# Kernel optimization log

Measured on AMD Instinct MI355X. Metric: run time of the kernel, lower is better.

## Reference

```python
import jax, jax.numpy as jnp
import numpy as np

B, T, U, D = 32, 128, 768, 768


def setup_inputs() -> dict:
    key = jax.random.key(0)
    ks = jax.random.split(key, 8)
    s = 0.02  # init scale for kernels (glorot-ish for 768)
    return {
        "x": jax.random.normal(ks[0], (B, T, D), jnp.float32),
        "h0": jax.random.normal(ks[1], (B, U), jnp.float32) * 0.1,
        "kernel": jax.random.normal(ks[2], (U, D), jnp.float32) * s,
        "recurrent_kernel": jax.random.normal(ks[3], (U, U), jnp.float32) * s,
        "attention_kernel": jax.random.normal(ks[4], (U, D), jnp.float32) * s,
        "recurrent_attention_kernel": jax.random.normal(ks[5], (U, U), jnp.float32) * s,
        "bias": jnp.zeros((U,), jnp.float32),
        "gamma_prime_attention": jnp.float32(-1.0),
        "gamma_prime_recurrent_attention": jnp.float32(-1.0),
    }


def _cell(x_t, h, kernel, rk, ak, rak, bias, ga, gra):
    # x_t: [B,D], h: [B,U]
    # input cross-attention: outer(h, x_t) * ak, exp, row-normalize, gate by kernel
    att = jnp.exp(h[:, :, None] * x_t[:, None, :] * ak)          # [B,U,D]
    att = att / jnp.sum(att, axis=-1, keepdims=True)
    att = att * kernel                                            # [B,U,D]
    hh = x_t @ kernel.T                                           # [B,U]
    hh = hh + ga * jnp.einsum('bud,bd->bu', att, x_t)
    hh = hh + bias
    # recurrent self-attention: outer(h, h) * rak, exp, row-normalize, gate by rk
    ratt = jnp.exp(h[:, :, None] * h[:, None, :] * rak)           # [B,U,U]
    ratt = ratt / jnp.sum(ratt, axis=-1, keepdims=True)
    ratt = ratt * rk
    out = hh + h @ rk.T + gra * jnp.einsum('buv,bv->bu', ratt, h)
    return jnp.tanh(out)


def reference(x, h0, kernel, recurrent_kernel, attention_kernel,
              recurrent_attention_kernel, bias,
              gamma_prime_attention, gamma_prime_recurrent_attention):
    ga = jax.nn.sigmoid(gamma_prime_attention)
    gra = jax.nn.sigmoid(gamma_prime_recurrent_attention)

    def step(h, x_t):
        o = _cell(x_t, h, kernel, recurrent_kernel, attention_kernel,
                  recurrent_attention_kernel, bias, ga, gra)
        return o, o

    _, ys = jax.lax.scan(step, h0, jnp.swapaxes(x, 0, 1))  # ys: [T,B,U]
    return jnp.swapaxes(ys, 0, 1)  # [B,T,U]
```

## Files before the change

### kernel.cpp

```cpp
#include <hip/hip_runtime.h>

#define NB 32
#define NT 128
#define NU 768
#define ND 768
#define UPB 3
#define NBLK (NU / UPB)
#define NTHR (256 * UPB)

#define AGENT __HIP_MEMORY_SCOPE_AGENT

__device__ __forceinline__ float fexp2(float x) { return __builtin_amdgcn_exp2f(x); }
__device__ __forceinline__ float frcp(float x)  { return __builtin_amdgcn_rcpf(x); }

__global__ void transpose_x_kernel(const float* __restrict__ x, float* __restrict__ xT) {
  __shared__ float tile[32][33];
  const int t  = blockIdx.x;
  const int d0 = blockIdx.y * 32;
  const int lo = threadIdx.x & 31;
  const int hi = threadIdx.x >> 5;
#pragma unroll
  for (int bb = hi; bb < 32; bb += 8)
    tile[bb][lo] = x[((size_t)bb * NT + t) * ND + d0 + lo];
  __syncthreads();
#pragma unroll
  for (int dd = hi; dd < 32; dd += 8)
    xT[((size_t)t * ND + d0 + dd) * NB + lo] = tile[lo][dd];
}

__global__ void init_h_kernel(const float* __restrict__ h0, float* __restrict__ hT,
                              unsigned int* __restrict__ flags) {
  int i = blockIdx.x * 256 + threadIdx.x;
  if (i < NU * NB) hT[i] = h0[(i & 31) * NU + (i >> 5)];
  if (i < NBLK) flags[i] = 0u;
}

__global__ void transpose_out_kernel(const float* __restrict__ outT, float* __restrict__ out) {
  __shared__ float tile[32][33];
  const int t  = blockIdx.x;
  const int u0 = blockIdx.y * 32;
  const int lo = threadIdx.x & 31;
  const int hi = threadIdx.x >> 5;
#pragma unroll
  for (int uu = hi; uu < 32; uu += 8)
    tile[uu][lo] = outT[((size_t)t * NU + u0 + uu) * NB + lo];
  __syncthreads();
#pragma unroll
  for (int bb = hi; bb < 32; bb += 8)
    out[((size_t)bb * NT + t) * NU + u0 + lo] = tile[lo][bb];
}

__global__ void __launch_bounds__(NTHR)
rnn_fused_kernel(const float* __restrict__ xT,
                 const float* __restrict__ wk,
                 const float* __restrict__ wrk,
                 const float* __restrict__ wak,
                 const float* __restrict__ wrak,
                 const float* __restrict__ bias,
                 const float* __restrict__ gpa,
                 const float* __restrict__ gpra,
                 float* hA, float* hB,
                 float* __restrict__ outT,
                 unsigned int* flags)
{
  const int tid  = threadIdx.x;
  const int uloc = tid >> 8;
  const int lt   = tid & 255;
  const int b    = lt & 31;
  const int c    = lt >> 5;
  const int d0   = c * 96;
  const int u    = blockIdx.x * UPB + uloc;

  __shared__ float2 s2a[UPB][ND];
  __shared__ float2 s2r[UPB][ND];
  __shared__ float  red[UPB][6][4][32];

#pragma unroll
  for (int j = 0; j < UPB; ++j) {
    const int ug = blockIdx.x * UPB + j;
    s2a[j][tid] = make_float2(wak [(size_t)ug * ND + tid], wk [(size_t)ug * ND + tid]);
    s2r[j][tid] = make_float2(wrak[(size_t)ug * NU + tid], wrk[(size_t)ug * NU + tid]);
  }
  const float bias_u = bias[u];
  const float ga  = 1.0f / (1.0f + __expf(-gpa[0]));
  const float gra = 1.0f / (1.0f + __expf(-gpra[0]));
  __syncthreads();

  float* hcur  = hA;
  float* hnext = hB;
  const float LOG2E = 1.4426950408889634f;

  for (int t = 0; t < NT; ++t) {
    const float hu = __hip_atomic_load(&hcur[u * NB + b], __ATOMIC_RELAXED, AGENT);
    const float hs = hu * LOG2E;

    float s_a = 0.f, n_a = 0.f, l_a = 0.f;
    {
      const float*  xp = xT + ((size_t)t * ND + d0) * NB + b;
      const float2* wa = &s2a[uloc][d0];
#pragma unroll 8
      for (int k = 0; k < 96; ++k) {
        float2 w2 = wa[k];
        float  xv = xp[k * NB];
        float  e  = fexp2(hs * xv * w2.x);
        float  kx = w2.y * xv;
        s_a += e;
        l_a += kx;
        n_a = fmaf(e, kx, n_a);
      }
    }
    float s_r = 0.f, n_r = 0.f, l_r = 0.f;
    {
      float*        hp = hcur + (size_t)d0 * NB + b;
      const float2* wr = &s2r[uloc][d0];
#pragma unroll 8
      for (int k = 0; k < 96; ++k) {
        float2 w2 = wr[k];
        float  hv = __hip_atomic_load(&hp[k * NB], __ATOMIC_RELAXED, AGENT);
        float  e  = fexp2(hs * hv * w2.x);
        float  kh = w2.y * hv;
        s_r += e;
        l_r += kh;
        n_r = fmaf(e, kh, n_r);
      }
    }

    float v0 = s_a + __shfl_xor(s_a, 32);
    float v1 = n_a + __shfl_xor(n_a, 32);
    float v2 = l_a + __shfl_xor(l_a, 32);
    float v3 = s_r + __shfl_xor(s_r, 32);
    float v4 = n_r + __shfl_xor(n_r, 32);
    float v5 = l_r + __shfl_xor(l_r, 32);
    const int w = (tid >> 6) & 3;
    if ((tid & 63) < 32) {
      red[uloc][0][w][b] = v0; red[uloc][1][w][b] = v1; red[uloc][2][w][b] = v2;
      red[uloc][3][w][b] = v3; red[uloc][4][w][b] = v4; red[uloc][5][w][b] = v5;
    }
    __syncthreads();

    if (lt < 32) {
      float r0 = red[uloc][0][0][b] + red[uloc][0][1][b] + red[uloc][0][2][b] + red[uloc][0][3][b];
      float r1 = red[uloc][1][0][b] + red[uloc][1][1][b] + red[uloc][1][2][b] + red[uloc][1][3][b];
      float r2 = red[uloc][2][0][b] + red[uloc][2][1][b] + red[uloc][2][2][b] + red[uloc][2][3][b];
      float r3 = red[uloc][3][0][b] + red[uloc][3][1][b] + red[uloc][3][2][b] + red[uloc][3][3][b];
      float r4 = red[uloc][4][0][b] + red[uloc][4][1][b] + red[uloc][4][2][b] + red[uloc][4][3][b];
      float r5 = red[uloc][5][0][b] + red[uloc][5][1][b] + red[uloc][5][2][b] + red[uloc][5][3][b];
      float hh = r2 + bias_u + ga * (r1 * frcp(r0));
      float z  = hh + r5 + gra * (r4 * frcp(r3));
      float ex = fexp2(z * 2.8853900817779268f);
      float o  = 1.0f - 2.0f * frcp(ex + 1.0f);
      __hip_atomic_store(&hnext[u * NB + b], o, __ATOMIC_RELAXED, AGENT);
      outT[((size_t)t * NU + u) * NB + b] = o;
    }

    if (t != NT - 1) {
      asm volatile("s_waitcnt vmcnt(0)" ::: "memory");
      __syncthreads();
      if (tid == 0)
        __hip_atomic_store(&flags[blockIdx.x], (unsigned)(t + 1), __ATOMIC_RELAXED, AGENT);
      if (tid < NBLK) {
        const unsigned tgt = (unsigned)(t + 1);
        while (__hip_atomic_load(&flags[tid], __ATOMIC_RELAXED, AGENT) < tgt)
          __builtin_amdgcn_s_sleep(2);
      }
      __syncthreads();
    }
    { float* tmp = hcur; hcur = hnext; hnext = tmp; }
  }
}

extern "C" void kernel_launch(void* const* d_in, const int* in_sizes, int n_in,
                              void* d_out, int out_size, void* d_ws, size_t ws_size,
                              hipStream_t stream) {
  const float* x    = (const float*)d_in[0];
  const float* h0   = (const float*)d_in[1];
  const float* wk   = (const float*)d_in[2];
  const float* wrk  = (const float*)d_in[3];
  const float* wak  = (const float*)d_in[4];
  const float* wrak = (const float*)d_in[5];
  const float* bias = (const float*)d_in[6];
  const float* gpa  = (const float*)d_in[7];
  const float* gpra = (const float*)d_in[8];
  float* out = (float*)d_out;

  float* xT   = (float*)d_ws;
  float* outT = xT + (size_t)NT * ND * NB;
  float* hA   = outT + (size_t)NT * NU * NB;
  float* hB   = hA + NU * NB;
  unsigned int* flags = (unsigned int*)(hB + NU * NB);

  transpose_x_kernel<<<dim3(NT, ND / 32), 256, 0, stream>>>(x, xT);
  init_h_kernel<<<(NU * NB + 255) / 256, 256, 0, stream>>>(h0, hA, flags);
  rnn_fused_kernel<<<NBLK, NTHR, 0, stream>>>(xT, wk, wrk, wak, wrak, bias, gpa, gpra,
                                              hA, hB, outT, flags);
  transpose_out_kernel<<<dim3(NT, NU / 32), 256, 0, stream>>>(outT, out);
}
```

Baseline: 1.997 ms.

## Stage hidden state in LDS per step and vectorize the inner loops

Each step, the block now cooperatively loads the whole hidden state (stored batch-major) into padded shared memory with dwordx4 loads that bypass stale cache (sc1). The inner loop then reads h from LDS instead of issuing per-element atomic global loads. x is also relaid out so each thread reads contiguous 96-float chunks, and the weights are split into separate arrays, so the two attention loops fuse into one loop using 128-bit loads. This is meant to cut global-memory latency on the critical serial recurrence, at the cost of about 99KB of extra LDS and a full per-step h broadcast into every block.

```diff
diff --git a/kernel.cpp b/kernel.cpp
--- a/kernel.cpp
+++ b/kernel.cpp
@@ -7,31 +7,28 @@
 #define UPB 3
 #define NBLK (NU / UPB)
 #define NTHR (256 * UPB)
+#define HPAD 772
 
 #define AGENT __HIP_MEMORY_SCOPE_AGENT
+
+typedef float f32x4 __attribute__((ext_vector_type(4)));
 
 __device__ __forceinline__ float fexp2(float x) { return __builtin_amdgcn_exp2f(x); }
 __device__ __forceinline__ float frcp(float x)  { return __builtin_amdgcn_rcpf(x); }
 
-__global__ void transpose_x_kernel(const float* __restrict__ x, float* __restrict__ xT) {
-  __shared__ float tile[32][33];
-  const int t  = blockIdx.x;
-  const int d0 = blockIdx.y * 32;
-  const int lo = threadIdx.x & 31;
-  const int hi = threadIdx.x >> 5;
-#pragma unroll
-  for (int bb = hi; bb < 32; bb += 8)
-    tile[bb][lo] = x[((size_t)bb * NT + t) * ND + d0 + lo];
-  __syncthreads();
-#pragma unroll
-  for (int dd = hi; dd < 32; dd += 8)
-    xT[((size_t)t * ND + d0 + dd) * NB + lo] = tile[lo][dd];
+__global__ void make_xc_kernel(const float* __restrict__ x, float* __restrict__ xc) {
+  const int t = blockIdx.x;
+  const int c = blockIdx.y;
+  for (int e = threadIdx.x; e < 32 * 96; e += 256) {
+    int b = e / 96, k = e - b * 96;
+    xc[(((size_t)t * 8 + c) * 32) * 96 + e] = x[((size_t)b * NT + t) * ND + c * 96 + k];
+  }
 }
 
 __global__ void init_h_kernel(const float* __restrict__ h0, float* __restrict__ hT,
                               unsigned int* __restrict__ flags) {
   int i = blockIdx.x * 256 + threadIdx.x;
-  if (i < NU * NB) hT[i] = h0[(i & 31) * NU + (i >> 5)];
+  if (i < NU * NB) hT[i] = h0[i];
   if (i < NBLK) flags[i] = 0u;
 }
 
@@ -50,8 +47,8 @@
     out[((size_t)bb * NT + t) * NU + u0 + lo] = tile[lo][bb];
 }
 
-__global__ void __launch_bounds__(NTHR)
-rnn_fused_kernel(const float* __restrict__ xT,
+__global__ void __launch_bounds__(NTHR, 3)
+rnn_fused_kernel(const float* __restrict__ xc,
                  const float* __restrict__ wk,
                  const float* __restrict__ wrk,
                  const float* __restrict__ wak,
@@ -59,7 +56,7 @@
                  const float* __restrict__ bias,
                  const float* __restrict__ gpa,
                  const float* __restrict__ gpra,
-                 float* hA, float* hB,
+                 float* hTA, float* hTB,
                  float* __restrict__ outT,
                  unsigned int* flags)
 {
@@ -71,57 +68,72 @@
   const int d0   = c * 96;
   const int u    = blockIdx.x * UPB + uloc;
 
-  __shared__ float2 s2a[UPB][ND];
-  __shared__ float2 s2r[UPB][ND];
-  __shared__ float  red[UPB][6][4][32];
+  __shared__ __align__(16) float s_ak[UPB][ND], s_k[UPB][ND], s_rak[UPB][ND], s_rk[UPB][ND];
+  __shared__ __align__(16) float sh[NB * HPAD];
+  __shared__ float red[UPB][6][4][32];
 
 #pragma unroll
   for (int j = 0; j < UPB; ++j) {
     const int ug = blockIdx.x * UPB + j;
-    s2a[j][tid] = make_float2(wak [(size_t)ug * ND + tid], wk [(size_t)ug * ND + tid]);
-    s2r[j][tid] = make_float2(wrak[(size_t)ug * NU + tid], wrk[(size_t)ug * NU + tid]);
+    s_ak [j][tid] = wak [(size_t)ug * ND + tid];
+    s_k  [j][tid] = wk  [(size_t)ug * ND + tid];
+    s_rak[j][tid] = wrak[(size_t)ug * NU + tid];
+    s_rk [j][tid] = wrk [(size_t)ug * NU + tid];
   }
   const float bias_u = bias[u];
   const float ga  = 1.0f / (1.0f + __expf(-gpa[0]));
   const float gra = 1.0f / (1.0f + __expf(-gpra[0]));
-  __syncthreads();
-
-  float* hcur  = hA;
-  float* hnext = hB;
+
+  const int tq = tid / 192;
+  const int ur = 4 * tid - 768 * tq;
+
+  const float* hcurT = hTA;
+  float* hnextT = hTB;
   const float LOG2E = 1.4426950408889634f;
 
   for (int t = 0; t < NT; ++t) {
-    const float hu = __hip_atomic_load(&hcur[u * NB + b], __ATOMIC_RELAXED, AGENT);
+    f32x4 hr[8];
+#pragma unroll
+    for (int j = 0; j < 8; ++j) {
+      const float* p = hcurT + j * 3072 + 4 * tid;
+      asm volatile("global_load_dwordx4 %0, %1, off sc1"
+                   : "=&v"(hr[j]) : "v"(p) : "memory");
+    }
+    asm volatile("s_waitcnt vmcnt(0)" ::: "memory");
+    __builtin_amdgcn_sched_barrier(0);
+#pragma unroll
+    for (int j = 0; j < 8; ++j)
+      *(f32x4*)&sh[(4 * j + tq) * HPAD + ur] = hr[j];
+    __syncthreads();
+
+    const float hu = sh[b * HPAD + u];
     const float hs = hu * LOG2E;
 
     float s_a = 0.f, n_a = 0.f, l_a = 0.f;
-    {
-      const float*  xp = xT + ((size_t)t * ND + d0) * NB + b;
-      const float2* wa = &s2a[uloc][d0];
-#pragma unroll 8
-      for (int k = 0; k < 96; ++k) {
-        float2 w2 = wa[k];
-        float  xv = xp[k * NB];
-        float  e  = fexp2(hs * xv * w2.x);
-        float  kx = w2.y * xv;
-        s_a += e;
-        l_a += kx;
-        n_a = fmaf(e, kx, n_a);
-      }
-    }
     float s_r = 0.f, n_r = 0.f, l_r = 0.f;
-    {
-      float*        hp = hcur + (size_t)d0 * NB + b;
-      const float2* wr = &s2r[uloc][d0];
-#pragma unroll 8
-      for (int k = 0; k < 96; ++k) {
-        float2 w2 = wr[k];
-        float  hv = __hip_atomic_load(&hp[k * NB], __ATOMIC_RELAXED, AGENT);
-        float  e  = fexp2(hs * hv * w2.x);
-        float  kh = w2.y * hv;
-        s_r += e;
-        l_r += kh;
-        n_r = fmaf(e, kh, n_r);
+    const float* xp  = xc + ((size_t)(t * 8 + c) * 32 + b) * 96;
+    const float* hp  = &sh[b * HPAD + d0];
+    const float* ap  = &s_ak [uloc][d0];
+    const float* kp  = &s_k  [uloc][d0];
+    const float* rap = &s_rak[uloc][d0];
+    const float* rkp = &s_rk [uloc][d0];
+
+#pragma unroll 4
+    for (int k4 = 0; k4 < 24; ++k4) {
+      f32x4 xv  = *(const f32x4*)(xp  + 4 * k4);
+      f32x4 hv  = *(const f32x4*)(hp  + 4 * k4);
+      f32x4 av  = *(const f32x4*)(ap  + 4 * k4);
+      f32x4 kv  = *(const f32x4*)(kp  + 4 * k4);
+      f32x4 rav = *(const f32x4*)(rap + 4 * k4);
+      f32x4 rkv = *(const f32x4*)(rkp + 4 * k4);
+#pragma unroll
+      for (int j = 0; j < 4; ++j) {
+        float e  = fexp2(hs * xv[j] * av[j]);
+        float kx = kv[j] * xv[j];
+        s_a += e; l_a += kx; n_a = fmaf(e, kx, n_a);
+        float er = fexp2(hs * hv[j] * rav[j]);
+        float kh = rkv[j] * hv[j];
+        s_r += er; l_r += kh; n_r = fmaf(er, kh, n_r);
       }
     }
 
@@ -149,7 +161,7 @@
       float z  = hh + r5 + gra * (r4 * frcp(r3));
       float ex = fexp2(z * 2.8853900817779268f);
       float o  = 1.0f - 2.0f * frcp(ex + 1.0f);
-      __hip_atomic_store(&hnext[u * NB + b], o, __ATOMIC_RELAXED, AGENT);
+      __hip_atomic_store(&hnextT[b * NU + u], o, __ATOMIC_RELAXED, AGENT);
       outT[((size_t)t * NU + u) * NB + b] = o;
     }
 
@@ -165,7 +177,7 @@
       }
       __syncthreads();
     }
-    { float* tmp = hcur; hcur = hnext; hnext = tmp; }
+    { const float* tmp = hcurT; hcurT = hnextT; hnextT = (float*)tmp; }
   }
 }
 
@@ -183,15 +195,15 @@
   const float* gpra = (const float*)d_in[8];
   float* out = (float*)d_out;
 
-  float* xT   = (float*)d_ws;
-  float* outT = xT + (size_t)NT * ND * NB;
-  float* hA   = outT + (size_t)NT * NU * NB;
-  float* hB   = hA + NU * NB;
-  unsigned int* flags = (unsigned int*)(hB + NU * NB);
-
-  transpose_x_kernel<<<dim3(NT, ND / 32), 256, 0, stream>>>(x, xT);
-  init_h_kernel<<<(NU * NB + 255) / 256, 256, 0, stream>>>(h0, hA, flags);
-  rnn_fused_kernel<<<NBLK, NTHR, 0, stream>>>(xT, wk, wrk, wak, wrak, bias, gpa, gpra,
-                                              hA, hB, outT, flags);
+  float* xc   = (float*)d_ws;
+  float* outT = xc + (size_t)NT * ND * NB;
+  float* hTA  = outT + (size_t)NT * NU * NB;
+  float* hTB  = hTA + NU * NB;
+  unsigned int* flags = (unsigned int*)(hTB + NU * NB);
+
+  make_xc_kernel<<<dim3(NT, 8), 256, 0, stream>>>(x, xc);
+  init_h_kernel<<<(NU * NB + 255) / 256, 256, 0, stream>>>(h0, hTA, flags);
+  rnn_fused_kernel<<<NBLK, NTHR, 0, stream>>>(xc, wk, wrk, wak, wrak, bias, gpa, gpra,
+                                              hTA, hTB, outT, flags);
   transpose_out_kernel<<<dim3(NT, NU / 32), 256, 0, stream>>>(outT, out);
 }
```

After: 2.202 ms. 10.3% more time.

## Split the batch across two blocks per unit group to double block count

Applied to the files above, without the earlier changes.

Each group of three hidden units is now handled by two blocks, one per half of the batch, giving 512 blocks in total. Each thread reduces over 48 features instead of 96, and an extra shuffle stage folds the sixteen chunks. This halves the serial work per thread at every time step, which is meant to shorten the per-step critical path. In exchange the grid-wide flag barrier now polls 512 flags, each block loads the full weight rows, global loads are only 16 floats wide, and all 512 blocks must be co-resident or the spin barrier deadlocks.

```diff
diff --git a/kernel.cpp b/kernel.cpp
--- a/kernel.cpp
+++ b/kernel.cpp
@@ -5,8 +5,10 @@
 #define NU 768
 #define ND 768
 #define UPB 3
-#define NBLK (NU / UPB)
-#define NTHR (256 * UPB)
+#define NC 16
+#define CL 48
+#define NBLK 512
+#define NTHR 768
 
 #define AGENT __HIP_MEMORY_SCOPE_AGENT
 
@@ -50,7 +52,7 @@
     out[((size_t)bb * NT + t) * NU + u0 + lo] = tile[lo][bb];
 }
 
-__global__ void __launch_bounds__(NTHR)
+__global__ void __launch_bounds__(NTHR, 6)
 rnn_fused_kernel(const float* __restrict__ xT,
                  const float* __restrict__ wk,
                  const float* __restrict__ wrk,
@@ -63,21 +65,24 @@
                  float* __restrict__ outT,
                  unsigned int* flags)
 {
-  const int tid  = threadIdx.x;
-  const int uloc = tid >> 8;
-  const int lt   = tid & 255;
-  const int b    = lt & 31;
-  const int c    = lt >> 5;
-  const int d0   = c * 96;
-  const int u    = blockIdx.x * UPB + uloc;
+  const int tid   = threadIdx.x;
+  const int uloc  = tid >> 8;
+  const int lt    = tid & 255;
+  const int b     = lt & 15;
+  const int c     = lt >> 4;
+  const int d0    = c * CL;
+  const int ugrp  = blockIdx.x >> 1;
+  const int bhalf = blockIdx.x & 1;
+  const int u     = ugrp * UPB + uloc;
+  const int bg    = bhalf * 16 + b;
 
   __shared__ float2 s2a[UPB][ND];
   __shared__ float2 s2r[UPB][ND];
-  __shared__ float  red[UPB][6][4][32];
+  __shared__ float  red[UPB][6][4][16];
 
 #pragma unroll
   for (int j = 0; j < UPB; ++j) {
-    const int ug = blockIdx.x * UPB + j;
+    const int ug = ugrp * UPB + j;
     s2a[j][tid] = make_float2(wak [(size_t)ug * ND + tid], wk [(size_t)ug * ND + tid]);
     s2r[j][tid] = make_float2(wrak[(size_t)ug * NU + tid], wrk[(size_t)ug * NU + tid]);
   }
@@ -91,66 +96,62 @@
   const float LOG2E = 1.4426950408889634f;
 
   for (int t = 0; t < NT; ++t) {
-    const float hu = __hip_atomic_load(&hcur[u * NB + b], __ATOMIC_RELAXED, AGENT);
+    const float hu = __hip_atomic_load(&hcur[u * NB + bg], __ATOMIC_RELAXED, AGENT);
     const float hs = hu * LOG2E;
 
     float s_a = 0.f, n_a = 0.f, l_a = 0.f;
     {
-      const float*  xp = xT + ((size_t)t * ND + d0) * NB + b;
+      const float*  xp = xT + ((size_t)t * ND + d0) * NB + bg;
       const float2* wa = &s2a[uloc][d0];
 #pragma unroll 8
-      for (int k = 0; k < 96; ++k) {
+      for (int k = 0; k < CL; ++k) {
         float2 w2 = wa[k];
         float  xv = xp[k * NB];
         float  e  = fexp2(hs * xv * w2.x);
         float  kx = w2.y * xv;
-        s_a += e;
-        l_a += kx;
-        n_a = fmaf(e, kx, n_a);
+        s_a += e; l_a += kx; n_a = fmaf(e, kx, n_a);
       }
     }
     float s_r = 0.f, n_r = 0.f, l_r = 0.f;
     {
-      float*        hp = hcur + (size_t)d0 * NB + b;
+      float*        hp = hcur + (size_t)d0 * NB + bg;
       const float2* wr = &s2r[uloc][d0];
 #pragma unroll 8
-      for (int k = 0; k < 96; ++k) {
+      for (int k = 0; k < CL; ++k) {
         float2 w2 = wr[k];
         float  hv = __hip_atomic_load(&hp[k * NB], __ATOMIC_RELAXED, AGENT);
         float  e  = fexp2(hs * hv * w2.x);
         float  kh = w2.y * hv;
-        s_r += e;
-        l_r += kh;
-        n_r = fmaf(e, kh, n_r);
+        s_r += e; l_r += kh; n_r = fmaf(e, kh, n_r);
       }
     }
 
-    float v0 = s_a + __shfl_xor(s_a, 32);
-    float v1 = n_a + __shfl_xor(n_a, 32);
-    float v2 = l_a + __shfl_xor(l_a, 32);
-    float v3 = s_r + __shfl_xor(s_r, 32);
-    float v4 = n_r + __shfl_xor(n_r, 32);
-    float v5 = l_r + __shfl_xor(l_r, 32);
-    const int w = (tid >> 6) & 3;
-    if ((tid & 63) < 32) {
+    float v0 = s_a, v1 = n_a, v2 = l_a, v3 = s_r, v4 = n_r, v5 = l_r;
+    v0 += __shfl_xor(v0, 32); v1 += __shfl_xor(v1, 32); v2 += __shfl_xor(v2, 32);
+    v3 += __shfl_xor(v3, 32); v4 += __shfl_xor(v4, 32); v5 += __shfl_xor(v5, 32);
+    v0 += __shfl_xor(v0, 16); v1 += __shfl_xor(v1, 16); v2 += __shfl_xor(v2, 16);
+    v3 += __shfl_xor(v3, 16); v4 += __shfl_xor(v4, 16); v5 += __shfl_xor(v5, 16);
+    const int w = c >> 2;
+    if ((tid & 63) < 16) {
       red[uloc][0][w][b] = v0; red[uloc][1][w][b] = v1; red[uloc][2][w][b] = v2;
       red[uloc][3][w][b] = v3; red[uloc][4][w][b] = v4; red[uloc][5][w][b] = v5;
     }
     __syncthreads();
 
-    if (lt < 32) {
-      float r0 = red[uloc][0][0][b] + red[uloc][0][1][b] + red[uloc][0][2][b] + red[uloc][0][3][b];
-      float r1 = red[uloc][1][0][b] + red[uloc][1][1][b] + red[uloc][1][2][b] + red[uloc][1][3][b];
-      float r2 = red[uloc][2][0][b] + red[uloc][2][1][b] + red[uloc][2][2][b] + red[uloc][2][3][b];
-      float r3 = red[uloc][3][0][b] + red[uloc][3][1][b] + red[uloc][3][2][b] + red[uloc][3][3][b];
-      float r4 = red[uloc][4][0][b] + red[uloc][4][1][b] + red[uloc][4][2][b] + red[uloc][4][3][b];
-      float r5 = red[uloc][5][0][b] + red[uloc][5][1][b] + red[uloc][5][2][b] + red[uloc][5][3][b];
+    if (lt < 16) {
+      float r0 = red[uloc][0][0][lt] + red[uloc][0][1][lt] + red[uloc][0][2][lt] + red[uloc][0][3][lt];
+      float r1 = red[uloc][1][0][lt] + red[uloc][1][1][lt] + red[uloc][1][2][lt] + red[uloc][1][3][lt];
+      float r2 = red[uloc][2][0][lt] + red[uloc][2][1][lt] + red[uloc][2][2][lt] + red[uloc][2][3][lt];
+      float r3 = red[uloc][3][0][lt] + red[uloc][3][1][lt] + red[uloc][3][2][lt] + red[uloc][3][3][lt];
+      float r4 = red[uloc][4][0][lt] + red[uloc][4][1][lt] + red[uloc][4][2][lt] + red[uloc][4][3][lt];
+      float r5 = red[uloc][5][0][lt] + red[uloc][5][1][lt] + red[uloc][5][2][lt] + red[uloc][5][3][lt];
+      const int bgl = bhalf * 16 + lt;
       float hh = r2 + bias_u + ga * (r1 * frcp(r0));
       float z  = hh + r5 + gra * (r4 * frcp(r3));
       float ex = fexp2(z * 2.8853900817779268f);
       float o  = 1.0f - 2.0f * frcp(ex + 1.0f);
-      __hip_atomic_store(&hnext[u * NB + b], o, __ATOMIC_RELAXED, AGENT);
-      outT[((size_t)t * NU + u) * NB + b] = o;
+      __hip_atomic_store(&hnext[u * NB + bgl], o, __ATOMIC_RELAXED, AGENT);
+      outT[((size_t)t * NU + u) * NB + bgl] = o;
     }
 
     if (t != NT - 1) {
```

Measured after the change: 2.619 ms. 31.2% more time.

## Vectorize RNN step with 4-wide packed x/h layout and two batches per thread

Applied to the files above, without the earlier changes.

Replaces the transposed x and h layouts with a packed [d/4][b][4] format so each thread loads four consecutive d values with 16-byte vector loads, and h with 8-byte atomic loads. Each thread now handles two batch rows and 48 d elements instead of one row and 96. Weights are split into separate LDS arrays read as float4, and the reductions become a wider two-level shuffle plus LDS reduce. The aim is fewer load instructions and more reuse of LDS weight reads per step, at the cost of more registers and extra shuffle work.

```diff
diff --git a/kernel.cpp b/kernel.cpp
--- a/kernel.cpp
+++ b/kernel.cpp
@@ -5,33 +5,37 @@
 #define NU 768
 #define ND 768
 #define UPB 3
-#define NBLK (NU / UPB)
-#define NTHR (256 * UPB)
+#define NBLK 256
+#define NTHR 768
 
 #define AGENT __HIP_MEMORY_SCOPE_AGENT
+
+typedef float f32x2 __attribute__((ext_vector_type(2)));
+typedef float f32x4 __attribute__((ext_vector_type(4)));
 
 __device__ __forceinline__ float fexp2(float x) { return __builtin_amdgcn_exp2f(x); }
 __device__ __forceinline__ float frcp(float x)  { return __builtin_amdgcn_rcpf(x); }
-
-__global__ void transpose_x_kernel(const float* __restrict__ x, float* __restrict__ xT) {
-  __shared__ float tile[32][33];
-  const int t  = blockIdx.x;
-  const int d0 = blockIdx.y * 32;
-  const int lo = threadIdx.x & 31;
-  const int hi = threadIdx.x >> 5;
-#pragma unroll
-  for (int bb = hi; bb < 32; bb += 8)
-    tile[bb][lo] = x[((size_t)bb * NT + t) * ND + d0 + lo];
-  __syncthreads();
-#pragma unroll
-  for (int dd = hi; dd < 32; dd += 8)
-    xT[((size_t)t * ND + d0 + dd) * NB + lo] = tile[lo][dd];
-}
-
-__global__ void init_h_kernel(const float* __restrict__ h0, float* __restrict__ hT,
-                              unsigned int* __restrict__ flags) {
+__device__ __forceinline__ int h4idx(int u, int b) { return ((u >> 2) * 32 + b) * 4 + (u & 3); }
+
+__global__ void make_x4_kernel(const float* __restrict__ x, float* __restrict__ x4) {
+  const int t = blockIdx.x;
+  const int g = blockIdx.y;
+  const size_t obase = ((size_t)t * 192 + g * 32) * 128;
+#pragma unroll
+  for (int i = 0; i < 16; ++i) {
+    int o = i * 256 + threadIdx.x;
+    int d4l = o >> 7, b = (o >> 2) & 31, j = o & 3;
+    x4[obase + o] = x[((size_t)b * NT + t) * ND + (g * 32 + d4l) * 4 + j];
+  }
+}
+
+__global__ void init_h4_kernel(const float* __restrict__ h0, float* __restrict__ h4,
+                               unsigned int* __restrict__ flags) {
   int i = blockIdx.x * 256 + threadIdx.x;
-  if (i < NU * NB) hT[i] = h0[(i & 31) * NU + (i >> 5)];
+  if (i < NU * NB) {
+    int u4 = i >> 7, b = (i >> 2) & 31, j = i & 3;
+    h4[i] = h0[b * NU + u4 * 4 + j];
+  }
   if (i < NBLK) flags[i] = 0u;
 }
 
@@ -50,8 +54,8 @@
     out[((size_t)bb * NT + t) * NU + u0 + lo] = tile[lo][bb];
 }
 
-__global__ void __launch_bounds__(NTHR)
-rnn_fused_kernel(const float* __restrict__ xT,
+__global__ void __launch_bounds__(NTHR, 3)
+rnn_fused_kernel(const float* __restrict__ x4,
                  const float* __restrict__ wk,
                  const float* __restrict__ wrk,
                  const float* __restrict__ wak,
@@ -66,91 +70,146 @@
   const int tid  = threadIdx.x;
   const int uloc = tid >> 8;
   const int lt   = tid & 255;
-  const int b    = lt & 31;
-  const int c    = lt >> 5;
-  const int d0   = c * 96;
+  const int b    = lt & 15;
+  const int c    = lt >> 4;
+  const int d0   = c * 48;
   const int u    = blockIdx.x * UPB + uloc;
 
-  __shared__ float2 s2a[UPB][ND];
-  __shared__ float2 s2r[UPB][ND];
-  __shared__ float  red[UPB][6][4][32];
+  __shared__ __align__(16) float s_ak[UPB][ND], s_k[UPB][ND], s_rak[UPB][ND], s_rk[UPB][ND];
+  __shared__ float red[UPB][12][4][16];
 
 #pragma unroll
   for (int j = 0; j < UPB; ++j) {
     const int ug = blockIdx.x * UPB + j;
-    s2a[j][tid] = make_float2(wak [(size_t)ug * ND + tid], wk [(size_t)ug * ND + tid]);
-    s2r[j][tid] = make_float2(wrak[(size_t)ug * NU + tid], wrk[(size_t)ug * NU + tid]);
+    s_ak [j][tid] = wak [(size_t)ug * ND + tid];
+    s_k  [j][tid] = wk  [(size_t)ug * ND + tid];
+    s_rak[j][tid] = wrak[(size_t)ug * NU + tid];
+    s_rk [j][tid] = wrk [(size_t)ug * NU + tid];
   }
   const float bias_u = bias[u];
   const float ga  = 1.0f / (1.0f + __expf(-gpa[0]));
   const float gra = 1.0f / (1.0f + __expf(-gpra[0]));
   __syncthreads();
 
-  float* hcur  = hA;
+  const float* hcur = hA;
   float* hnext = hB;
   const float LOG2E = 1.4426950408889634f;
 
   for (int t = 0; t < NT; ++t) {
-    const float hu = __hip_atomic_load(&hcur[u * NB + b], __ATOMIC_RELAXED, AGENT);
-    const float hs = hu * LOG2E;
-
-    float s_a = 0.f, n_a = 0.f, l_a = 0.f;
-    {
-      const float*  xp = xT + ((size_t)t * ND + d0) * NB + b;
-      const float2* wa = &s2a[uloc][d0];
-#pragma unroll 8
-      for (int k = 0; k < 96; ++k) {
-        float2 w2 = wa[k];
-        float  xv = xp[k * NB];
-        float  e  = fexp2(hs * xv * w2.x);
-        float  kx = w2.y * xv;
-        s_a += e;
-        l_a += kx;
-        n_a = fmaf(e, kx, n_a);
-      }
-    }
-    float s_r = 0.f, n_r = 0.f, l_r = 0.f;
-    {
-      float*        hp = hcur + (size_t)d0 * NB + b;
-      const float2* wr = &s2r[uloc][d0];
-#pragma unroll 8
-      for (int k = 0; k < 96; ++k) {
-        float2 w2 = wr[k];
-        float  hv = __hip_atomic_load(&hp[k * NB], __ATOMIC_RELAXED, AGENT);
-        float  e  = fexp2(hs * hv * w2.x);
-        float  kh = w2.y * hv;
-        s_r += e;
-        l_r += kh;
-        n_r = fmaf(e, kh, n_r);
-      }
-    }
-
-    float v0 = s_a + __shfl_xor(s_a, 32);
-    float v1 = n_a + __shfl_xor(n_a, 32);
-    float v2 = l_a + __shfl_xor(l_a, 32);
-    float v3 = s_r + __shfl_xor(s_r, 32);
-    float v4 = n_r + __shfl_xor(n_r, 32);
-    float v5 = l_r + __shfl_xor(l_r, 32);
+    const float huA = __hip_atomic_load(&hcur[h4idx(u, b)],      __ATOMIC_RELAXED, AGENT);
+    const float huB = __hip_atomic_load(&hcur[h4idx(u, b + 16)], __ATOMIC_RELAXED, AGENT);
+    const float hsA = huA * LOG2E, hsB = huB * LOG2E;
+    const f32x4 hsA4 = {hsA, hsA, hsA, hsA};
+    const f32x4 hsB4 = {hsB, hsB, hsB, hsB};
+
+    f32x4 saA = {0,0,0,0}, naA = {0,0,0,0}, laA = {0,0,0,0};
+    f32x4 srA = {0,0,0,0}, nrA = {0,0,0,0}, lrA = {0,0,0,0};
+    f32x4 saB = {0,0,0,0}, naB = {0,0,0,0}, laB = {0,0,0,0};
+    f32x4 srB = {0,0,0,0}, nrB = {0,0,0,0}, lrB = {0,0,0,0};
+
+    const f32x4*  xp = (const f32x4*)x4 + (((size_t)t * 192 + c * 12) * 32 + b);
+    const double* hq = (const double*)hcur + ((size_t)(c * 12) * 32 + b) * 2;
+
+#pragma unroll
+    for (int k4 = 0; k4 < 12; ++k4) {
+      const f32x4 av  = *(const f32x4*)&s_ak [uloc][d0 + 4 * k4];
+      const f32x4 kv  = *(const f32x4*)&s_k  [uloc][d0 + 4 * k4];
+      const f32x4 rav = *(const f32x4*)&s_rak[uloc][d0 + 4 * k4];
+      const f32x4 rkv = *(const f32x4*)&s_rk [uloc][d0 + 4 * k4];
+      const f32x4 xvA = xp[k4 * 32];
+      const f32x4 xvB = xp[k4 * 32 + 16];
+      const double hdA0 = __hip_atomic_load(hq + (size_t)k4 * 64,      __ATOMIC_RELAXED, AGENT);
+      const double hdA1 = __hip_atomic_load(hq + (size_t)k4 * 64 + 1,  __ATOMIC_RELAXED, AGENT);
+      const double hdB0 = __hip_atomic_load(hq + (size_t)k4 * 64 + 32, __ATOMIC_RELAXED, AGENT);
+      const double hdB1 = __hip_atomic_load(hq + (size_t)k4 * 64 + 33, __ATOMIC_RELAXED, AGENT);
+      const f32x2 ha0 = __builtin_bit_cast(f32x2, hdA0);
+      const f32x2 ha1 = __builtin_bit_cast(f32x2, hdA1);
+      const f32x2 hb0 = __builtin_bit_cast(f32x2, hdB0);
+      const f32x2 hb1 = __builtin_bit_cast(f32x2, hdB1);
+      const f32x4 hvA = {ha0.x, ha0.y, ha1.x, ha1.y};
+      const f32x4 hvB = {hb0.x, hb0.y, hb1.x, hb1.y};
+
+      f32x4 tA = (xvA * av) * hsA4;
+      f32x4 tB = (xvB * av) * hsB4;
+      f32x4 eA = {fexp2(tA.x), fexp2(tA.y), fexp2(tA.z), fexp2(tA.w)};
+      f32x4 eB = {fexp2(tB.x), fexp2(tB.y), fexp2(tB.z), fexp2(tB.w)};
+      f32x4 kxA = kv * xvA;
+      f32x4 kxB = kv * xvB;
+      saA += eA; laA += kxA; naA += eA * kxA;
+      saB += eB; laB += kxB; naB += eB * kxB;
+
+      f32x4 rtA = (hvA * rav) * hsA4;
+      f32x4 rtB = (hvB * rav) * hsB4;
+      f32x4 reA = {fexp2(rtA.x), fexp2(rtA.y), fexp2(rtA.z), fexp2(rtA.w)};
+      f32x4 reB = {fexp2(rtB.x), fexp2(rtB.y), fexp2(rtB.z), fexp2(rtB.w)};
+      f32x4 khA = rkv * hvA;
+      f32x4 khB = rkv * hvB;
+      srA += reA; lrA += khA; nrA += reA * khA;
+      srB += reB; lrB += khB; nrB += reB * khB;
+    }
+
+    float v0  = saA.x + saA.y + saA.z + saA.w;
+    float v1  = naA.x + naA.y + naA.z + naA.w;
+    float v2  = laA.x + laA.y + laA.z + laA.w;
+    float v3  = srA.x + srA.y + srA.z + srA.w;
+    float v4  = nrA.x + nrA.y + nrA.z + nrA.w;
+    float v5  = lrA.x + lrA.y + lrA.z + lrA.w;
+    float v6  = saB.x + saB.y + saB.z + saB.w;
+    float v7  = naB.x + naB.y + naB.z + naB.w;
+    float v8  = laB.x + laB.y + laB.z + laB.w;
+    float v9  = srB.x + srB.y + srB.z + srB.w;
+    float v10 = nrB.x + nrB.y + nrB.z + nrB.w;
+    float v11 = lrB.x + lrB.y + lrB.z + lrB.w;
+
+    v0  += __shfl_xor(v0, 16);  v0  += __shfl_xor(v0, 32);
+    v1  += __shfl_xor(v1, 16);  v1  += __shfl_xor(v1, 32);
+    v2  += __shfl_xor(v2, 16);  v2  += __shfl_xor(v2, 32);
+    v3  += __shfl_xor(v3, 16);  v3  += __shfl_xor(v3, 32);
+    v4  += __shfl_xor(v4, 16);  v4  += __shfl_xor(v4, 32);
+    v5  += __shfl_xor(v5, 16);  v5  += __shfl_xor(v5, 32);
+    v6  += __shfl_xor(v6, 16);  v6  += __shfl_xor(v6, 32);
+    v7  += __shfl_xor(v7, 16);  v7  += __shfl_xor(v7, 32);
+    v8  += __shfl_xor(v8, 16);  v8  += __shfl_xor(v8, 32);
+    v9  += __shfl_xor(v9, 16);  v9  += __shfl_xor(v9, 32);
+    v10 += __shfl_xor(v10, 16); v10 += __shfl_xor(v10, 32);
+    v11 += __shfl_xor(v11, 16); v11 += __shfl_xor(v11, 32);
+
     const int w = (tid >> 6) & 3;
-    if ((tid & 63) < 32) {
-      red[uloc][0][w][b] = v0; red[uloc][1][w][b] = v1; red[uloc][2][w][b] = v2;
-      red[uloc][3][w][b] = v3; red[uloc][4][w][b] = v4; red[uloc][5][w][b] = v5;
+    if ((tid & 63) < 16) {
+      red[uloc][0][w][b] = v0;   red[uloc][1][w][b] = v1;   red[uloc][2][w][b] = v2;
+      red[uloc][3][w][b] = v3;   red[uloc][4][w][b] = v4;   red[uloc][5][w][b] = v5;
+      red[uloc][6][w][b] = v6;   red[uloc][7][w][b] = v7;   red[uloc][8][w][b] = v8;
+      red[uloc][9][w][b] = v9;   red[uloc][10][w][b] = v10; red[uloc][11][w][b] = v11;
     }
     __syncthreads();
 
-    if (lt < 32) {
-      float r0 = red[uloc][0][0][b] + red[uloc][0][1][b] + red[uloc][0][2][b] + red[uloc][0][3][b];
-      float r1 = red[uloc][1][0][b] + red[uloc][1][1][b] + red[uloc][1][2][b] + red[uloc][1][3][b];
-      float r2 = red[uloc][2][0][b] + red[uloc][2][1][b] + red[uloc][2][2][b] + red[uloc][2][3][b];
-      float r3 = red[uloc][3][0][b] + red[uloc][3][1][b] + red[uloc][3][2][b] + red[uloc][3][3][b];
-      float r4 = red[uloc][4][0][b] + red[uloc][4][1][b] + red[uloc][4][2][b] + red[uloc][4][3][b];
-      float r5 = red[uloc][5][0][b] + red[uloc][5][1][b] + red[uloc][5][2][b] + red[uloc][5][3][b];
-      float hh = r2 + bias_u + ga * (r1 * frcp(r0));
-      float z  = hh + r5 + gra * (r4 * frcp(r3));
-      float ex = fexp2(z * 2.8853900817779268f);
-      float o  = 1.0f - 2.0f * frcp(ex + 1.0f);
-      __hip_atomic_store(&hnext[u * NB + b], o, __ATOMIC_RELAXED, AGENT);
-      outT[((size_t)t * NU + u) * NB + b] = o;
+    if (lt < 16) {
+      float r0  = red[uloc][0][0][lt]  + red[uloc][0][1][lt]  + red[uloc][0][2][lt]  + red[uloc][0][3][lt];
+      float r1  = red[uloc][1][0][lt]  + red[uloc][1][1][lt]  + red[uloc][1][2][lt]  + red[uloc][1][3][lt];
+      float r2  = red[uloc][2][0][lt]  + red[uloc][2][1][lt]  + red[uloc][2][2][lt]  + red[uloc][2][3][lt];
+      float r3  = red[uloc][3][0][lt]  + red[uloc][3][1][lt]  + red[uloc][3][2][lt]  + red[uloc][3][3][lt];
+      float r4  = red[uloc][4][0][lt]  + red[uloc][4][1][lt]  + red[uloc][4][2][lt]  + red[uloc][4][3][lt];
+      float r5  = red[uloc][5][0][lt]  + red[uloc][5][1][lt]  + red[uloc][5][2][lt]  + red[uloc][5][3][lt];
+      float r6  = red[uloc][6][0][lt]  + red[uloc][6][1][lt]  + red[uloc][6][2][lt]  + red[uloc][6][3][lt];
+      float r7  = red[uloc][7][0][lt]  + red[uloc][7][1][lt]  + red[uloc][7][2][lt]  + red[uloc][7][3][lt];
+      float r8  = red[uloc][8][0][lt]  + red[uloc][8][1][lt]  + red[uloc][8][2][lt]  + red[uloc][8][3][lt];
+      float r9  = red[uloc][9][0][lt]  + red[uloc][9][1][lt]  + red[uloc][9][2][lt]  + red[uloc][9][3][lt];
+      float r10 = red[uloc][10][0][lt] + red[uloc][10][1][lt] + red[uloc][10][2][lt] + red[uloc][10][3][lt];
+      float r11 = red[uloc][11][0][lt] + red[uloc][11][1][lt] + red[uloc][11][2][lt] + red[uloc][11][3][lt];
+
+      float hhA = r2 + bias_u + ga * (r1 * frcp(r0));
+      float zA  = hhA + r5 + gra * (r4 * frcp(r3));
+      float exA = fexp2(zA * 2.8853900817779268f);
+      float oA  = 1.0f - 2.0f * frcp(exA + 1.0f);
+      float hhB = r8 + bias_u + ga * (r7 * frcp(r6));
+      float zB  = hhB + r11 + gra * (r10 * frcp(r9));
+      float exB = fexp2(zB * 2.8853900817779268f);
+      float oB  = 1.0f - 2.0f * frcp(exB + 1.0f);
+
+      __hip_atomic_store(&hnext[h4idx(u, lt)],      oA, __ATOMIC_RELAXED, AGENT);
+      __hip_atomic_store(&hnext[h4idx(u, lt + 16)], oB, __ATOMIC_RELAXED, AGENT);
+      outT[((size_t)t * NU + u) * NB + lt]      = oA;
+      outT[((size_t)t * NU + u) * NB + lt + 16] = oB;
     }
 
     if (t != NT - 1) {
@@ -165,7 +224,7 @@
       }
       __syncthreads();
     }
-    { float* tmp = hcur; hcur = hnext; hnext = tmp; }
+    { const float* tmp = hcur; hcur = hnext; hnext = (float*)tmp; }
   }
 }
 
@@ -183,15 +242,15 @@
   const float* gpra = (const float*)d_in[8];
   float* out = (float*)d_out;
 
-  float* xT   = (float*)d_ws;
-  float* outT = xT + (size_t)NT * ND * NB;
+  float* x4   = (float*)d_ws;
+  float* outT = x4 + (size_t)NT * ND * NB;
   float* hA   = outT + (size_t)NT * NU * NB;
   float* hB   = hA + NU * NB;
   unsigned int* flags = (unsigned int*)(hB + NU * NB);
 
-  transpose_x_kernel<<<dim3(NT, ND / 32), 256, 0, stream>>>(x, xT);
-  init_h_kernel<<<(NU * NB + 255) / 256, 256, 0, stream>>>(h0, hA, flags);
-  rnn_fused_kernel<<<NBLK, NTHR, 0, stream>>>(xT, wk, wrk, wak, wrak, bias, gpa, gpra,
+  make_x4_kernel<<<dim3(NT, 6), 256, 0, stream>>>(x, x4);
+  init_h4_kernel<<<(NU * NB + 255) / 256, 256, 0, stream>>>(h0, hA, flags);
+  rnn_fused_kernel<<<NBLK, NTHR, 0, stream>>>(x4, wk, wrk, wak, wrak, bias, gpa, gpra,
                                               hA, hB, outT, flags);
   transpose_out_kernel<<<dim3(NT, NU / 32), 256, 0, stream>>>(outT, out);
 }
```

New measurement: 1.835 ms. -8.1%, faster.
